# Optimization experiments

Measured on AMD Instinct MI355X. Metric: run time of the kernel, lower is better.

## Reference

```python
import jax, jax.numpy as jnp
import numpy as np

B, H, S, DH = 2, 16, 2048, 64


def _decay_matrix(num_heads, seqlen):
    # RetNet per-head decay: gamma_h = 1 - 2^{-5-h}, D[h,n,m] = gamma_h^{n-m} for n>=m else 0
    h = np.arange(num_heads)
    gamma = 1.0 - 2.0 ** (-5.0 - h)  # [H]
    n = np.arange(seqlen)[:, None]
    m = np.arange(seqlen)[None, :]
    diff = (n - m).astype(np.float32)  # [S,S]
    D = np.where(diff >= 0, gamma[:, None, None] ** diff[None, :, :], 0.0)
    D = np.nan_to_num(D, nan=0.0)
    return jnp.asarray(D, dtype=jnp.float32)


def setup_inputs() -> dict:
    key = jax.random.key(0)
    kq, kk, kv = jax.random.split(key, 3)
    Q = jax.random.normal(kq, (B, H, S, DH), dtype=jnp.float32)
    K = jax.random.normal(kk, (B, H, S, DH), dtype=jnp.float32)
    V = jax.random.normal(kv, (B, H, S, DH), dtype=jnp.float32)
    D = _decay_matrix(H, S)  # [H,S,S]
    return {"Q": Q, "K": K, "V": V, "D": D}


def reference(Q, K, V, D):
    # scores = Q @ K^T : [B,H,S,S]
    scores = jnp.einsum("bhqd,bhkd->bhqk", Q, K)
    # retention: elementwise decay mask (no softmax), broadcast D over batch
    MSR = scores * D[None, :, :, :]
    out = jnp.einsum("bhqk,bhkd->bhqd", MSR, V)
    return (out, MSR)
```

## Files before the change

kernel.cpp:

```cpp
#include <hip/hip_runtime.h>
#include <hip/hip_bf16.h>
#include <math.h>

#define S_LEN 2048
#define DHEAD 64
#define NHEADS 16
#define NBATCH 2
#define TM 64
#define TN 64
#define LDSS 68
#define NTHR 256

typedef __attribute__((ext_vector_type(4))) float f32x4;
typedef __attribute__((ext_vector_type(4))) short s16x4;
typedef __attribute__((ext_vector_type(8))) short s16x8;

static __device__ __forceinline__ short f2bf(float f) {
    union { float f; unsigned u; } x; x.f = f;
    unsigned r = (x.u + 0x7fffu + ((x.u >> 16) & 1u)) >> 16;
    return (short)r;
}

static __device__ __forceinline__ s16x8 ld_frag(const short* p) {
    const s16x4* p4 = (const s16x4*)p;
    s16x4 lo = p4[0], hi = p4[1];
    s16x8 r;
    r[0]=lo[0]; r[1]=lo[1]; r[2]=lo[2]; r[3]=lo[3];
    r[4]=hi[0]; r[5]=hi[1]; r[6]=hi[2]; r[7]=hi[3];
    return r;
}

__global__ __launch_bounds__(NTHR, 4)
void retnet_fused(const float* __restrict__ Q, const float* __restrict__ K,
                  const float* __restrict__ V, float* __restrict__ out,
                  float* __restrict__ msr) {
    __shared__ short Qs[TM * LDSS];
    __shared__ short Ks[TN * LDSS];
    __shared__ short Vts[DHEAD * LDSS];
    __shared__ short Ps[TM * LDSS];

    const int t   = blockIdx.x;
    const int bh  = blockIdx.y;
    const int h   = bh & (NHEADS - 1);
    const int tid = threadIdx.x;
    const int w   = tid >> 6;
    const int l   = tid & 63;
    const int n0  = t * TM;

    const float* Qp = Q + (size_t)bh * S_LEN * DHEAD;
    const float* Kp = K + (size_t)bh * S_LEN * DHEAD;
    const float* Vp = V + (size_t)bh * S_LEN * DHEAD;
    float* outp = out + (size_t)bh * S_LEN * DHEAD;
    float* msrp = msr + (size_t)bh * S_LEN * S_LEN;

    const float gamma = 1.0f - exp2f(-5.0f - (float)h);
    const float log2g = (float)log2((double)gamma);

    #pragma unroll
    for (int p = 0; p < 4; ++p) {
        int idx = p * NTHR + tid;
        int row = idx >> 4;
        int c4  = (idx & 15) << 2;
        f32x4 q = *(const f32x4*)(Qp + (n0 + row) * DHEAD + c4);
        s16x4 qb; qb[0]=f2bf(q[0]); qb[1]=f2bf(q[1]); qb[2]=f2bf(q[2]); qb[3]=f2bf(q[3]);
        *(s16x4*)(&Qs[row * LDSS + c4]) = qb;
    }

    f32x4 accO[4];
    #pragma unroll
    for (int c = 0; c < 4; ++c) accO[c] = (f32x4){0.f,0.f,0.f,0.f};

    const int colid = l & 15;
    const int quad  = l >> 4;
    const int arow  = (w << 4) + colid;
    const int k0    = quad << 3;

    for (int mt = 0; mt <= t; ++mt) {
        const int m0 = mt * TN;
        __syncthreads();

        #pragma unroll
        for (int p = 0; p < 4; ++p) {
            int idx = p * NTHR + tid;
            int row = idx >> 4;
            int c4  = (idx & 15) << 2;
            f32x4 k = *(const f32x4*)(Kp + (m0 + row) * DHEAD + c4);
            s16x4 kb; kb[0]=f2bf(k[0]); kb[1]=f2bf(k[1]); kb[2]=f2bf(k[2]); kb[3]=f2bf(k[3]);
            *(s16x4*)(&Ks[row * LDSS + c4]) = kb;
        }
        #pragma unroll
        for (int p = 0; p < 4; ++p) {
            int d0 = ((p << 2) + w) << 2;
            f32x4 v = *(const f32x4*)(Vp + (m0 + l) * DHEAD + d0);
            Vts[(d0 + 0) * LDSS + l] = f2bf(v[0]);
            Vts[(d0 + 1) * LDSS + l] = f2bf(v[1]);
            Vts[(d0 + 2) * LDSS + l] = f2bf(v[2]);
            Vts[(d0 + 3) * LDSS + l] = f2bf(v[3]);
        }
        __syncthreads();

        f32x4 accS[4];
        #pragma unroll
        for (int c = 0; c < 4; ++c) accS[c] = (f32x4){0.f,0.f,0.f,0.f};
        #pragma unroll
        for (int kc = 0; kc < 2; ++kc) {
            s16x8 a = ld_frag(&Qs[arow * LDSS + (kc << 5) + k0]);
            #pragma unroll
            for (int c = 0; c < 4; ++c) {
                s16x8 b = ld_frag(&Ks[((c << 4) + colid) * LDSS + (kc << 5) + k0]);
                accS[c] = __builtin_amdgcn_mfma_f32_16x16x32_bf16(a, b, accS[c], 0, 0, 0);
            }
        }

        #pragma unroll
        for (int c = 0; c < 4; ++c) {
            int mloc = (c << 4) + colid;
            int m = m0 + mloc;
            #pragma unroll
            for (int r = 0; r < 4; ++r) {
                int nloc = (w << 4) + (quad << 2) + r;
                int n = n0 + nloc;
                int delta = n - m;
                float dec = (delta >= 0) ? exp2f((float)delta * log2g) : 0.0f;
                float val = accS[c][r] * dec;
                msrp[n * S_LEN + m] = val;
                Ps[nloc * LDSS + mloc] = f2bf(val);
            }
        }
        __syncthreads();

        #pragma unroll
        for (int kc = 0; kc < 2; ++kc) {
            s16x8 a = ld_frag(&Ps[arow * LDSS + (kc << 5) + k0]);
            #pragma unroll
            for (int c = 0; c < 4; ++c) {
                s16x8 b = ld_frag(&Vts[((c << 4) + colid) * LDSS + (kc << 5) + k0]);
                accO[c] = __builtin_amdgcn_mfma_f32_16x16x32_bf16(a, b, accO[c], 0, 0, 0);
            }
        }
    }

    #pragma unroll
    for (int c = 0; c < 4; ++c) {
        int d = (c << 4) + colid;
        #pragma unroll
        for (int r = 0; r < 4; ++r) {
            int nloc = (w << 4) + (quad << 2) + r;
            outp[(n0 + nloc) * DHEAD + d] = accO[c][r];
        }
    }

    const int zc0 = (t + 1) * TN;
    const f32x4 z4 = (f32x4){0.f,0.f,0.f,0.f};
    for (int rr = 0; rr < TM; ++rr) {
        float* rowp = msrp + (n0 + rr) * S_LEN;
        for (int c4 = zc0 + (tid << 2); c4 < S_LEN; c4 += NTHR * 4) {
            *(f32x4*)(rowp + c4) = z4;
        }
    }
}

extern "C" void kernel_launch(void* const* d_in, const int* in_sizes, int n_in,
                              void* d_out, int out_size, void* d_ws, size_t ws_size,
                              hipStream_t stream) {
    const float* Q = (const float*)d_in[0];
    const float* K = (const float*)d_in[1];
    const float* V = (const float*)d_in[2];
    float* out = (float*)d_out;
    float* msr = out + (size_t)NBATCH * NHEADS * S_LEN * DHEAD;
    dim3 grid(S_LEN / TM, NBATCH * NHEADS);
    retnet_fused<<<grid, NTHR, 0, stream>>>(Q, K, V, out, msr);
}
```

Baseline: 956.9 us.

## Split key dimension into chunks across blocks with atomic output accumulation

```diff
diff --git a/kernel.cpp b/kernel.cpp
--- a/kernel.cpp
+++ b/kernel.cpp
@@ -8,6 +8,7 @@
 #define NBATCH 2
 #define TM 64
 #define TN 64
+#define CHUNK 8
 #define LDSS 68
 #define NTHR 256
 
@@ -30,6 +31,11 @@
     return r;
 }
 
+__global__ void zero_out_kernel(float* __restrict__ out) {
+    size_t i = (size_t)blockIdx.x * NTHR + threadIdx.x;
+    ((f32x4*)out)[i] = (f32x4){0.f, 0.f, 0.f, 0.f};
+}
+
 __global__ __launch_bounds__(NTHR, 4)
 void retnet_fused(const float* __restrict__ Q, const float* __restrict__ K,
                   const float* __restrict__ V, float* __restrict__ out,
@@ -40,12 +46,17 @@
     __shared__ short Ps[TM * LDSS];
 
     const int t   = blockIdx.x;
-    const int bh  = blockIdx.y;
+    const int ch  = blockIdx.y;
+    const int bh  = blockIdx.z;
     const int h   = bh & (NHEADS - 1);
     const int tid = threadIdx.x;
     const int w   = tid >> 6;
     const int l   = tid & 63;
     const int n0  = t * TM;
+
+    const int cbeg   = ch * CHUNK;
+    const int cend   = cbeg + CHUNK;
+    const int mt_end = (t + 1 < cend) ? (t + 1) : cend;
 
     const float* Qp = Q + (size_t)bh * S_LEN * DHEAD;
     const float* Kp = K + (size_t)bh * S_LEN * DHEAD;
@@ -56,106 +67,113 @@
     const float gamma = 1.0f - exp2f(-5.0f - (float)h);
     const float log2g = (float)log2((double)gamma);
 
-    #pragma unroll
-    for (int p = 0; p < 4; ++p) {
-        int idx = p * NTHR + tid;
-        int row = idx >> 4;
-        int c4  = (idx & 15) << 2;
-        f32x4 q = *(const f32x4*)(Qp + (n0 + row) * DHEAD + c4);
-        s16x4 qb; qb[0]=f2bf(q[0]); qb[1]=f2bf(q[1]); qb[2]=f2bf(q[2]); qb[3]=f2bf(q[3]);
-        *(s16x4*)(&Qs[row * LDSS + c4]) = qb;
-    }
-
-    f32x4 accO[4];
-    #pragma unroll
-    for (int c = 0; c < 4; ++c) accO[c] = (f32x4){0.f,0.f,0.f,0.f};
-
     const int colid = l & 15;
     const int quad  = l >> 4;
     const int arow  = (w << 4) + colid;
     const int k0    = quad << 3;
 
-    for (int mt = 0; mt <= t; ++mt) {
-        const int m0 = mt * TN;
-        __syncthreads();
-
+    if (cbeg < mt_end) {
         #pragma unroll
         for (int p = 0; p < 4; ++p) {
             int idx = p * NTHR + tid;
             int row = idx >> 4;
             int c4  = (idx & 15) << 2;
-            f32x4 k = *(const f32x4*)(Kp + (m0 + row) * DHEAD + c4);
-            s16x4 kb; kb[0]=f2bf(k[0]); kb[1]=f2bf(k[1]); kb[2]=f2bf(k[2]); kb[3]=f2bf(k[3]);
-            *(s16x4*)(&Ks[row * LDSS + c4]) = kb;
+            f32x4 q = *(const f32x4*)(Qp + (n0 + row) * DHEAD + c4);
+            s16x4 qb; qb[0]=f2bf(q[0]); qb[1]=f2bf(q[1]); qb[2]=f2bf(q[2]); qb[3]=f2bf(q[3]);
+            *(s16x4*)(&Qs[row * LDSS + c4]) = qb;
         }
+
+        f32x4 accO[4];
         #pragma unroll
-        for (int p = 0; p < 4; ++p) {
-            int d0 = ((p << 2) + w) << 2;
-            f32x4 v = *(const f32x4*)(Vp + (m0 + l) * DHEAD + d0);
-            Vts[(d0 + 0) * LDSS + l] = f2bf(v[0]);
-            Vts[(d0 + 1) * LDSS + l] = f2bf(v[1]);
-            Vts[(d0 + 2) * LDSS + l] = f2bf(v[2]);
-            Vts[(d0 + 3) * LDSS + l] = f2bf(v[3]);
-        }
-        __syncthreads();
+        for (int c = 0; c < 4; ++c) accO[c] = (f32x4){0.f,0.f,0.f,0.f};
 
-        f32x4 accS[4];
-        #pragma unroll
-        for (int c = 0; c < 4; ++c) accS[c] = (f32x4){0.f,0.f,0.f,0.f};
-        #pragma unroll
-        for (int kc = 0; kc < 2; ++kc) {
-            s16x8 a = ld_frag(&Qs[arow * LDSS + (kc << 5) + k0]);
+        for (int mt = cbeg; mt < mt_end; ++mt) {
+            const int m0 = mt * TN;
+            __syncthreads();
+
+            #pragma unroll
+            for (int p = 0; p < 4; ++p) {
+                int idx = p * NTHR + tid;
+                int row = idx >> 4;
+                int c4  = (idx & 15) << 2;
+                f32x4 k = *(const f32x4*)(Kp + (m0 + row) * DHEAD + c4);
+                s16x4 kb; kb[0]=f2bf(k[0]); kb[1]=f2bf(k[1]); kb[2]=f2bf(k[2]); kb[3]=f2bf(k[3]);
+                *(s16x4*)(&Ks[row * LDSS + c4]) = kb;
+            }
+            #pragma unroll
+            for (int p = 0; p < 4; ++p) {
+                int d0 = ((p << 2) + w) << 2;
+                f32x4 v = *(const f32x4*)(Vp + (m0 + l) * DHEAD + d0);
+                Vts[(d0 + 0) * LDSS + l] = f2bf(v[0]);
+                Vts[(d0 + 1) * LDSS + l] = f2bf(v[1]);
+                Vts[(d0 + 2) * LDSS + l] = f2bf(v[2]);
+                Vts[(d0 + 3) * LDSS + l] = f2bf(v[3]);
+            }
+            __syncthreads();
+
+            f32x4 accS[4];
+            #pragma unroll
+            for (int c = 0; c < 4; ++c) accS[c] = (f32x4){0.f,0.f,0.f,0.f};
+            #pragma unroll
+            for (int kc = 0; kc < 2; ++kc) {
+                s16x8 a = ld_frag(&Qs[arow * LDSS + (kc << 5) + k0]);
+                #pragma unroll
+                for (int c = 0; c < 4; ++c) {
+                    s16x8 b = ld_frag(&Ks[((c << 4) + colid) * LDSS + (kc << 5) + k0]);
+                    accS[c] = __builtin_amdgcn_mfma_f32_16x16x32_bf16(a, b, accS[c], 0, 0, 0);
+                }
+            }
+
             #pragma unroll
             for (int c = 0; c < 4; ++c) {
-                s16x8 b = ld_frag(&Ks[((c << 4) + colid) * LDSS + (kc << 5) + k0]);
-                accS[c] = __builtin_amdgcn_mfma_f32_16x16x32_bf16(a, b, accS[c], 0, 0, 0);
+                int mloc = (c << 4) + colid;
+                int m = m0 + mloc;
+                #pragma unroll
+                for (int r = 0; r < 4; ++r) {
+                    int nloc = (w << 4) + (quad << 2) + r;
+                    int n = n0 + nloc;
+                    int delta = n - m;
+                    float dec = (delta >= 0) ? exp2f((float)delta * log2g) : 0.0f;
+                    float val = accS[c][r] * dec;
+                    msrp[(size_t)n * S_LEN + m] = val;
+                    Ps[nloc * LDSS + mloc] = f2bf(val);
+                }
+            }
+            __syncthreads();
+
+            #pragma unroll
+            for (int kc = 0; kc < 2; ++kc) {
+                s16x8 a = ld_frag(&Ps[arow * LDSS + (kc << 5) + k0]);
+                #pragma unroll
+                for (int c = 0; c < 4; ++c) {
+                    s16x8 b = ld_frag(&Vts[((c << 4) + colid) * LDSS + (kc << 5) + k0]);
+                    accO[c] = __builtin_amdgcn_mfma_f32_16x16x32_bf16(a, b, accO[c], 0, 0, 0);
+                }
             }
         }
 
         #pragma unroll
         for (int c = 0; c < 4; ++c) {
-            int mloc = (c << 4) + colid;
-            int m = m0 + mloc;
+            int d = (c << 4) + colid;
             #pragma unroll
             for (int r = 0; r < 4; ++r) {
                 int nloc = (w << 4) + (quad << 2) + r;
-                int n = n0 + nloc;
-                int delta = n - m;
-                float dec = (delta >= 0) ? exp2f((float)delta * log2g) : 0.0f;
-                float val = accS[c][r] * dec;
-                msrp[n * S_LEN + m] = val;
-                Ps[nloc * LDSS + mloc] = f2bf(val);
-            }
-        }
-        __syncthreads();
-
-        #pragma unroll
-        for (int kc = 0; kc < 2; ++kc) {
-            s16x8 a = ld_frag(&Ps[arow * LDSS + (kc << 5) + k0]);
-            #pragma unroll
-            for (int c = 0; c < 4; ++c) {
-                s16x8 b = ld_frag(&Vts[((c << 4) + colid) * LDSS + (kc << 5) + k0]);
-                accO[c] = __builtin_amdgcn_mfma_f32_16x16x32_bf16(a, b, accO[c], 0, 0, 0);
+                unsafeAtomicAdd(&outp[(n0 + nloc) * DHEAD + d], accO[c][r]);
             }
         }
     }
 
-    #pragma unroll
-    for (int c = 0; c < 4; ++c) {
-        int d = (c << 4) + colid;
+    const int zbeg = (cbeg > t + 1) ? cbeg : (t + 1);
+    if (zbeg < cend) {
+        const int z0 = zbeg << 6;
+        const int z1 = cend << 6;
+        const f32x4 z4 = (f32x4){0.f,0.f,0.f,0.f};
         #pragma unroll
-        for (int r = 0; r < 4; ++r) {
-            int nloc = (w << 4) + (quad << 2) + r;
-            outp[(n0 + nloc) * DHEAD + d] = accO[c][r];
-        }
-    }
-
-    const int zc0 = (t + 1) * TN;
-    const f32x4 z4 = (f32x4){0.f,0.f,0.f,0.f};
-    for (int rr = 0; rr < TM; ++rr) {
-        float* rowp = msrp + (n0 + rr) * S_LEN;
-        for (int c4 = zc0 + (tid << 2); c4 < S_LEN; c4 += NTHR * 4) {
-            *(f32x4*)(rowp + c4) = z4;
+        for (int rp = 0; rp < 4; ++rp) {
+            float* rowp = msrp + (size_t)(n0 + (rp << 4) + (tid >> 4)) * S_LEN;
+            for (int cc = z0 + ((tid & 15) << 2); cc < z1; cc += 64) {
+                *(f32x4*)(rowp + cc) = z4;
+            }
         }
     }
 }
@@ -168,6 +186,10 @@
     const float* V = (const float*)d_in[2];
     float* out = (float*)d_out;
     float* msr = out + (size_t)NBATCH * NHEADS * S_LEN * DHEAD;
-    dim3 grid(S_LEN / TM, NBATCH * NHEADS);
+
+    const int o_elems = NBATCH * NHEADS * S_LEN * DHEAD;
+    zero_out_kernel<<<o_elems / 4 / NTHR, NTHR, 0, stream>>>(out);
+
+    dim3 grid(S_LEN / TM, S_LEN / TN / CHUNK, NBATCH * NHEADS);
     retnet_fused<<<grid, NTHR, 0, stream>>>(Q, K, V, out, msr);
 }
```

After: 788.7 us. 1.21x faster.
